# Optimization experiments

Hardware: AMD Instinct MI355X
Metric: run time of the kernel (lower is better)

The kernel has to match this reference:

```python
import jax, jax.numpy as jnp
import numpy as np

EMBED_DIM = 256
B, S = 4, 4096

def setup_inputs() -> dict:
    key = jax.random.key(0)
    k1, k2, k3, k4 = jax.random.split(key, 4)
    x = jax.random.normal(k1, (B, S, EMBED_DIM), dtype=jnp.float32)
    scale = 1.0 / np.sqrt(EMBED_DIM)
    Wq = jax.random.normal(k2, (EMBED_DIM, EMBED_DIM), dtype=jnp.float32) * scale
    Wk = jax.random.normal(k3, (EMBED_DIM, EMBED_DIM), dtype=jnp.float32) * scale
    Wv = jax.random.normal(k4, (EMBED_DIM, EMBED_DIM), dtype=jnp.float32) * scale
    return {"x": x, "Wq": Wq, "Wk": Wk, "Wv": Wv}

def reference(x, Wq, Wk, Wv):
    # nn.Linear: y = x @ W.T  (weights stored [out, in])
    Q = jnp.einsum('bse,oe->bso', x, Wq)
    K = jnp.einsum('bse,oe->bso', x, Wk)
    V = jnp.einsum('bse,oe->bso', x, Wv)
    inv_sqrt_d = 1.0 / np.sqrt(EMBED_DIM)
    scores = jnp.einsum('bqd,bkd->bqk', Q, K) * inv_sqrt_d  # [B,S,S]
    attn = jax.nn.softmax(scores, axis=-1)
    out = jnp.einsum('bqk,bkd->bqd', attn, V)
    return out
```

## Files before the change

kernel.cpp:

```cpp
#include <hip/hip_runtime.h>
#include <stdint.h>

#define SEQ   4096
#define EMB   256
#define NROW  16384

typedef short s16x8 __attribute__((ext_vector_type(8)));
typedef float f32x4 __attribute__((ext_vector_type(4)));

#define LOG2E 1.44269504088896340736f

__device__ __forceinline__ unsigned short f2bf(float f) {
    unsigned int u = __builtin_bit_cast(unsigned int, f);
    u += 0x7FFFu + ((u >> 16) & 1u);
    return (unsigned short)(u >> 16);
}

__device__ __forceinline__ void fence_barrier() {
    __asm__ volatile("s_waitcnt lgkmcnt(0)" ::: "memory");
    __builtin_amdgcn_s_barrier();
    __asm__ volatile("" ::: "memory");
}

__global__ __launch_bounds__(256, 8) void xcvt_kernel(
    const float* __restrict__ x, unsigned short* __restrict__ xb)
{
    const size_t i = (size_t)(blockIdx.x*256 + threadIdx.x) * 8;
    const float4 v0 = *(const float4*)(x + i);
    const float4 v1 = *(const float4*)(x + i + 4);
    union { unsigned short u[8]; s16x8 v; } o;
    o.u[0]=f2bf(v0.x); o.u[1]=f2bf(v0.y); o.u[2]=f2bf(v0.z); o.u[3]=f2bf(v0.w);
    o.u[4]=f2bf(v1.x); o.u[5]=f2bf(v1.y); o.u[6]=f2bf(v1.z); o.u[7]=f2bf(v1.w);
    *(s16x8*)(xb + i) = o.v;
}

#define PWSTR 264

__global__ __launch_bounds__(256, 2) void proj_kernel(
    const unsigned short* __restrict__ xb, const float* __restrict__ Wq,
    const float* __restrict__ Wk, const float* __restrict__ Wv,
    unsigned short* __restrict__ Qb, unsigned short* __restrict__ Kb,
    unsigned short* __restrict__ Vt)
{
    __shared__ unsigned short Wl[3][32][PWSTR];
    __shared__ unsigned short Vtr[32][72];
    const int bid = blockIdx.x;
    const int ct  = bid >> 6;
    const int rb  = bid & 63;
    const int t   = threadIdx.x;

    {
        const float* Ws[3] = {Wq, Wk, Wv};
        const int o = t >> 3, seg = t & 7;
        for (int w = 0; w < 3; ++w) {
            const float* src = Ws[w] + (ct*32 + o)*256 + seg*32;
            #pragma unroll
            for (int i = 0; i < 8; ++i) {
                float4 v = *(const float4*)(src + i*4);
                ushort4 bv;
                bv.x = f2bf(v.x); bv.y = f2bf(v.y); bv.z = f2bf(v.z); bv.w = f2bf(v.w);
                *(ushort4*)&Wl[w][o][seg*32 + i*4] = bv;
            }
        }
    }
    __syncthreads();

    const int wave = t >> 6, lane = t & 63;
    const int g = lane >> 4, lr = lane & 15;

    for (int it = 0; it < 4; ++it) {
        const int rowblk = rb*256 + it*64;
        const int rowbase = rowblk + wave*16;
        s16x8 a[8];
        {
            const unsigned short* xr = xb + (size_t)(rowbase + lr)*256;
            #pragma unroll
            for (int c = 0; c < 8; ++c)
                a[c] = *(const s16x8*)(xr + c*32 + g*8);
        }
        f32x4 acc[3][2];
        #pragma unroll
        for (int w = 0; w < 3; ++w)
            #pragma unroll
            for (int cf = 0; cf < 2; ++cf)
                #pragma unroll
                for (int j = 0; j < 4; ++j) acc[w][cf][j] = 0.0f;

        #pragma unroll
        for (int w = 0; w < 3; ++w)
            #pragma unroll
            for (int cf = 0; cf < 2; ++cf)
                #pragma unroll
                for (int c = 0; c < 8; ++c) {
                    s16x8 bfr = *(const s16x8*)&Wl[w][cf*16 + lr][c*32 + g*8];
                    acc[w][cf] = __builtin_amdgcn_mfma_f32_16x16x32_bf16(a[c], bfr, acc[w][cf], 0, 0, 0);
                }

        #pragma unroll
        for (int cf = 0; cf < 2; ++cf) {
            const int col = ct*32 + cf*16 + lr;
            #pragma unroll
            for (int j = 0; j < 4; ++j) {
                const int srow = rowbase + g*4 + j;
                Qb[(size_t)srow*256 + col] = f2bf(acc[0][cf][j] * 0.0625f);
                Kb[(size_t)srow*256 + col] = f2bf(acc[1][cf][j]);
            }
        }
        __syncthreads();
        #pragma unroll
        for (int cf = 0; cf < 2; ++cf) {
            ushort4 pv;
            pv.x = f2bf(acc[2][cf][0]); pv.y = f2bf(acc[2][cf][1]);
            pv.z = f2bf(acc[2][cf][2]); pv.w = f2bf(acc[2][cf][3]);
            *(ushort4*)&Vtr[cf*16 + lr][wave*16 + g*4] = pv;
        }
        __syncthreads();
        {
            const int colL = t >> 3, seg = t & 7;
            const int bb = rowblk >> 12, ss0 = rowblk & 4095;
            unsigned short* dst = Vt + ((size_t)(bb*256 + ct*32 + colL))*4096 + ss0 + seg*8;
            *(s16x8*)(dst) = *(const s16x8*)&Vtr[colL][seg*8];
        }
    }
}

#define KVB  32
#define NT   64
#define KSTR 264
#define VSTR 40
#define PSTR 40
#define RESCALE_THR 8.0f

__global__ __launch_bounds__(256, 2) void attn_kernel(
    const unsigned short* __restrict__ Qb, const unsigned short* __restrict__ Kb,
    const unsigned short* __restrict__ Vt, float* __restrict__ pacc0,
    float* __restrict__ pm, float* __restrict__ pl, float* __restrict__ out)
{
    __shared__ unsigned short Kl[2][KVB][KSTR];
    __shared__ unsigned short Vl[2][EMB][VSTR];
    __shared__ unsigned short Pl[4][16][PSTR];
    __shared__ float All[4][16];

    const int bid = blockIdx.x;
    const int grp = bid & 7;
    const int b = grp >> 1, h = grp & 1;
    const int qt  = bid >> 3;
    const int t   = threadIdx.x;
    const int wave = t >> 6, lane = t & 63;
    const int g = lane >> 4, lr = lane & 15;
    const int kv0 = h * 2048;
    const int rowbase = b*4096 + qt*64 + wave*16;

    s16x8 qa[8];
    {
        const unsigned short* qp = Qb + (size_t)(rowbase + lr)*256;
        #pragma unroll
        for (int c = 0; c < 8; ++c)
            qa[c] = *(const s16x8*)(qp + c*32 + g*8);
    }

    f32x4 acc[16];
    #pragma unroll
    for (int c = 0; c < 16; ++c)
        #pragma unroll
        for (int j = 0; j < 4; ++j) acc[c][j] = 0.0f;
    float m = -__builtin_inff(), l = 0.0f;

    const unsigned short* Kg = Kb + (size_t)b*4096*256;
    const unsigned short* Vg = Vt + (size_t)b*256*4096;

    s16x8 kreg[4], vreg[4];
    #pragma unroll
    for (int i = 0; i < 4; ++i) {
        const int idx = i*256 + t;
        const int kv = idx >> 5, e8 = idx & 31;
        kreg[i] = *(const s16x8*)(Kg + (size_t)(kv0 + kv)*256 + e8*8);
        const int d = idx >> 2, seg = idx & 3;
        vreg[i] = *(const s16x8*)(Vg + (size_t)d*4096 + kv0 + seg*8);
    }

    for (int kt = 0; kt < NT; ++kt) {
        const int buf = kt & 1;
        #pragma unroll
        for (int i = 0; i < 4; ++i) {
            const int idx = i*256 + t;
            const int kv = idx >> 5, e8 = idx & 31;
            *(s16x8*)&Kl[buf][kv][e8*8] = kreg[i];
            const int d = idx >> 2, seg = idx & 3;
            *(s16x8*)&Vl[buf][d][seg*8] = vreg[i];
        }
        if (kt + 1 < NT) {
            const int kvn = kv0 + (kt + 1) * KVB;
            #pragma unroll
            for (int i = 0; i < 4; ++i) {
                const int idx = i*256 + t;
                const int kv = idx >> 5, e8 = idx & 31;
                kreg[i] = *(const s16x8*)(Kg + (size_t)(kvn + kv)*256 + e8*8);
                const int d = idx >> 2, seg = idx & 3;
                vreg[i] = *(const s16x8*)(Vg + (size_t)d*4096 + kvn + seg*8);
            }
        }
        fence_barrier();

        f32x4 sc[2];
        #pragma unroll
        for (int f = 0; f < 2; ++f)
            #pragma unroll
            for (int j = 0; j < 4; ++j) sc[f][j] = 0.0f;
        __builtin_amdgcn_s_setprio(1);
        #pragma unroll
        for (int f = 0; f < 2; ++f)
            #pragma unroll
            for (int c = 0; c < 8; ++c) {
                s16x8 kb = *(const s16x8*)&Kl[buf][f*16 + lr][c*32 + g*8];
                sc[f] = __builtin_amdgcn_mfma_f32_16x16x32_bf16(kb, qa[c], sc[f], 0, 0, 0);
            }
        __builtin_amdgcn_s_setprio(0);

        float pmax = fmaxf(fmaxf(fmaxf(sc[0][0], sc[0][1]), fmaxf(sc[0][2], sc[0][3])),
                           fmaxf(fmaxf(sc[1][0], sc[1][1]), fmaxf(sc[1][2], sc[1][3])));
        pmax = fmaxf(pmax, __shfl_xor(pmax, 16));
        pmax = fmaxf(pmax, __shfl_xor(pmax, 32));

        if (!__all(pmax - m <= RESCALE_THR)) {
            const float mn = fmaxf(m, pmax);
            const float al = __builtin_amdgcn_exp2f((m - mn) * LOG2E);
            m = mn;
            l *= al;
            if (lane < 16) All[wave][lr] = al;
            f32x4 al4 = *(const f32x4*)&All[wave][g*4];
            #pragma unroll
            for (int c = 0; c < 16; ++c)
                #pragma unroll
                for (int j = 0; j < 4; ++j) acc[c][j] *= al4[j];
        }

        float p[2][4];
        #pragma unroll
        for (int f = 0; f < 2; ++f)
            #pragma unroll
            for (int j = 0; j < 4; ++j)
                p[f][j] = __builtin_amdgcn_exp2f((sc[f][j] - m) * LOG2E);
        float ps = (p[0][0] + p[0][1]) + (p[0][2] + p[0][3])
                 + (p[1][0] + p[1][1]) + (p[1][2] + p[1][3]);
        ps += __shfl_xor(ps, 16);
        ps += __shfl_xor(ps, 32);
        l += ps;

        ushort4 q0, q1;
        q0.x = f2bf(p[0][0]); q0.y = f2bf(p[0][1]); q0.z = f2bf(p[0][2]); q0.w = f2bf(p[0][3]);
        q1.x = f2bf(p[1][0]); q1.y = f2bf(p[1][1]); q1.z = f2bf(p[1][2]); q1.w = f2bf(p[1][3]);
        *(ushort4*)&Pl[wave][lr][g*4]      = q0;
        *(ushort4*)&Pl[wave][lr][16 + g*4] = q1;
        s16x8 pa = *(const s16x8*)&Pl[wave][lr][g*8];

        __builtin_amdgcn_s_setprio(1);
        #pragma unroll
        for (int c = 0; c < 16; ++c) {
            s16x8 vb = *(const s16x8*)&Vl[buf][c*16 + lr][g*8];
            acc[c] = __builtin_amdgcn_mfma_f32_16x16x32_bf16(pa, vb, acc[c], 0, 0, 0);
        }
        __builtin_amdgcn_s_setprio(0);
    }

    float* dst = h ? out : pacc0;
    #pragma unroll
    for (int c = 0; c < 16; ++c)
        #pragma unroll
        for (int j = 0; j < 4; ++j)
            dst[(size_t)(rowbase + g*4 + j)*256 + c*16 + lr] = acc[c][j];
    if (lane < 16) {
        pm[h*NROW + rowbase + lr] = m;
        pl[h*NROW + rowbase + lr] = l;
    }
}

__global__ __launch_bounds__(256, 4) void combine_kernel(
    const float* __restrict__ pacc0, const float* __restrict__ pm,
    const float* __restrict__ pl, float* __restrict__ out)
{
    const int idx = blockIdx.x*256 + threadIdx.x;
    const int row = idx >> 6, d4 = (idx & 63) << 2;
    const float m0 = pm[row], m1 = pm[NROW + row];
    const float l0 = pl[row], l1 = pl[NROW + row];
    const float M = fmaxf(m0, m1);
    const float w0 = __builtin_amdgcn_exp2f((m0 - M) * LOG2E);
    const float w1 = __builtin_amdgcn_exp2f((m1 - M) * LOG2E);
    const float r = 1.0f / (l0*w0 + l1*w1);
    const float4 a0 = *(const float4*)(pacc0 + (size_t)row*256 + d4);
    float4 a1 = *(const float4*)(out + (size_t)row*256 + d4);
    a1.x = (a0.x*w0 + a1.x*w1) * r;
    a1.y = (a0.y*w0 + a1.y*w1) * r;
    a1.z = (a0.z*w0 + a1.z*w1) * r;
    a1.w = (a0.w*w0 + a1.w*w1) * r;
    *(float4*)(out + (size_t)row*256 + d4) = a1;
}

extern "C" void kernel_launch(void* const* d_in, const int* in_sizes, int n_in,
                              void* d_out, int out_size, void* d_ws, size_t ws_size,
                              hipStream_t stream) {
    const float* x  = (const float*)d_in[0];
    const float* Wq = (const float*)d_in[1];
    const float* Wk = (const float*)d_in[2];
    const float* Wv = (const float*)d_in[3];

    unsigned short* Qb = (unsigned short*)d_ws;
    unsigned short* Kb = Qb + (size_t)NROW*EMB;
    unsigned short* Vt = Kb + (size_t)NROW*EMB;
    float* pacc0 = (float*)(Vt + (size_t)NROW*EMB);
    float* pm    = pacc0 + (size_t)NROW*EMB;
    float* pl    = pm + 2*NROW;
    unsigned short* xb = (unsigned short*)pacc0;

    xcvt_kernel<<<2048, 256, 0, stream>>>(x, xb);
    proj_kernel<<<512, 256, 0, stream>>>(xb, Wq, Wk, Wv, Qb, Kb, Vt);
    attn_kernel<<<512, 256, 0, stream>>>(Qb, Kb, Vt, pacc0, pm, pl, (float*)d_out);
    combine_kernel<<<4096, 256, 0, stream>>>(pacc0, pm, pl, (float*)d_out);
}
```

Measured before the change: 212.1 us.

## Rework attention to 32x32 MFMA with direct-to-LDS loads and intra-block KV split

The attention kernel moves to 512-thread blocks, each covering 128 query rows with 64-key tiles. Waves split the KV tile in half and merge their results in LDS at the end. It uses 32x32x16 bf16 MFMA, XOR-swizzled LDS staged through global_load_lds, and builds the P operand with cross-lane shuffles instead of an LDS round trip. The weight conversion to bf16 moves into the x-conversion kernel, and Q/K stores are coalesced through LDS in the projection kernel. The goals are fewer LDS round trips, fewer register-staged loads and better MFMA efficiency, at the cost of higher LDS use, a vmcnt(0) wait each tile and extra merge traffic.

```diff
diff --git a/kernel.cpp b/kernel.cpp
--- a/kernel.cpp
+++ b/kernel.cpp
@@ -5,10 +5,13 @@
 #define EMB   256
 #define NROW  16384
 
-typedef short s16x8 __attribute__((ext_vector_type(8)));
-typedef float f32x4 __attribute__((ext_vector_type(4)));
+typedef short s16x8  __attribute__((ext_vector_type(8)));
+typedef float f32x4  __attribute__((ext_vector_type(4)));
+typedef float f32x16 __attribute__((ext_vector_type(16)));
+typedef unsigned int u32;
 
 #define LOG2E 1.44269504088896340736f
+#define RESCALE_THR 8.0f
 
 __device__ __forceinline__ unsigned short f2bf(float f) {
     unsigned int u = __builtin_bit_cast(unsigned int, f);
@@ -16,33 +19,52 @@
     return (unsigned short)(u >> 16);
 }
 
-__device__ __forceinline__ void fence_barrier() {
-    __asm__ volatile("s_waitcnt lgkmcnt(0)" ::: "memory");
-    __builtin_amdgcn_s_barrier();
-    __asm__ volatile("" ::: "memory");
+__device__ __forceinline__ u32 pkbf2(float lo, float hi) {
+    return (u32)f2bf(lo) | ((u32)f2bf(hi) << 16);
+}
+
+typedef __attribute__((address_space(3))) u32 lds_u32;
+typedef __attribute__((address_space(1))) const u32 glb_u32;
+__device__ __forceinline__ void gload16(const unsigned short* g, const unsigned short* l) {
+    __builtin_amdgcn_global_load_lds((glb_u32*)(uintptr_t)g,
+                                     (lds_u32*)(u32)(uintptr_t)l, 16, 0, 0);
 }
 
 __global__ __launch_bounds__(256, 8) void xcvt_kernel(
-    const float* __restrict__ x, unsigned short* __restrict__ xb)
+    const float* __restrict__ x, const float* __restrict__ Wq,
+    const float* __restrict__ Wk, const float* __restrict__ Wv,
+    unsigned short* __restrict__ xb, unsigned short* __restrict__ Wb)
 {
-    const size_t i = (size_t)(blockIdx.x*256 + threadIdx.x) * 8;
-    const float4 v0 = *(const float4*)(x + i);
-    const float4 v1 = *(const float4*)(x + i + 4);
+    const int gid = blockIdx.x*256 + threadIdx.x;
+    const float* src;
+    unsigned short* dst;
+    size_t off;
+    if (gid < 524288) {
+        src = x; dst = xb; off = (size_t)gid * 8;
+    } else {
+        size_t wi = (size_t)(gid - 524288) * 8;
+        int w = (int)(wi >> 16);
+        off = wi & 65535;
+        src = (w == 0) ? Wq : (w == 1) ? Wk : Wv;
+        dst = Wb + (size_t)w * 65536;
+    }
+    const float4 v0 = *(const float4*)(src + off);
+    const float4 v1 = *(const float4*)(src + off + 4);
     union { unsigned short u[8]; s16x8 v; } o;
     o.u[0]=f2bf(v0.x); o.u[1]=f2bf(v0.y); o.u[2]=f2bf(v0.z); o.u[3]=f2bf(v0.w);
     o.u[4]=f2bf(v1.x); o.u[5]=f2bf(v1.y); o.u[6]=f2bf(v1.z); o.u[7]=f2bf(v1.w);
-    *(s16x8*)(xb + i) = o.v;
+    *(s16x8*)(dst + off) = o.v;
 }
 
 #define PWSTR 264
 
 __global__ __launch_bounds__(256, 2) void proj_kernel(
-    const unsigned short* __restrict__ xb, const float* __restrict__ Wq,
-    const float* __restrict__ Wk, const float* __restrict__ Wv,
+    const unsigned short* __restrict__ xb, const unsigned short* __restrict__ Wb,
     unsigned short* __restrict__ Qb, unsigned short* __restrict__ Kb,
     unsigned short* __restrict__ Vt)
 {
     __shared__ unsigned short Wl[3][32][PWSTR];
+    __shared__ unsigned short QKs[2][64][40];
     __shared__ unsigned short Vtr[32][72];
     const int bid = blockIdx.x;
     const int ct  = bid >> 6;
@@ -50,17 +72,13 @@
     const int t   = threadIdx.x;
 
     {
-        const float* Ws[3] = {Wq, Wk, Wv};
         const int o = t >> 3, seg = t & 7;
+        #pragma unroll
         for (int w = 0; w < 3; ++w) {
-            const float* src = Ws[w] + (ct*32 + o)*256 + seg*32;
-            #pragma unroll
-            for (int i = 0; i < 8; ++i) {
-                float4 v = *(const float4*)(src + i*4);
-                ushort4 bv;
-                bv.x = f2bf(v.x); bv.y = f2bf(v.y); bv.z = f2bf(v.z); bv.w = f2bf(v.w);
-                *(ushort4*)&Wl[w][o][seg*32 + i*4] = bv;
-            }
+            const unsigned short* src = Wb + (size_t)w*65536 + (ct*32 + o)*256 + seg*32;
+            #pragma unroll
+            for (int i = 0; i < 4; ++i)
+                *(s16x8*)&Wl[w][o][seg*32 + i*8] = *(const s16x8*)(src + i*8);
         }
     }
     __syncthreads();
@@ -96,19 +114,15 @@
                     acc[w][cf] = __builtin_amdgcn_mfma_f32_16x16x32_bf16(a[c], bfr, acc[w][cf], 0, 0, 0);
                 }
 
+        __syncthreads();
         #pragma unroll
         for (int cf = 0; cf < 2; ++cf) {
-            const int col = ct*32 + cf*16 + lr;
             #pragma unroll
             for (int j = 0; j < 4; ++j) {
-                const int srow = rowbase + g*4 + j;
-                Qb[(size_t)srow*256 + col] = f2bf(acc[0][cf][j] * 0.0625f);
-                Kb[(size_t)srow*256 + col] = f2bf(acc[1][cf][j]);
+                const int row = wave*16 + g*4 + j;
+                QKs[0][row][cf*16 + lr] = f2bf(acc[0][cf][j] * 0.0625f);
+                QKs[1][row][cf*16 + lr] = f2bf(acc[1][cf][j]);
             }
-        }
-        __syncthreads();
-        #pragma unroll
-        for (int cf = 0; cf < 2; ++cf) {
             ushort4 pv;
             pv.x = f2bf(acc[2][cf][0]); pv.y = f2bf(acc[2][cf][1]);
             pv.z = f2bf(acc[2][cf][2]); pv.w = f2bf(acc[2][cf][3]);
@@ -116,162 +130,190 @@
         }
         __syncthreads();
         {
+            const int row = t >> 2, cs = t & 3;
+            *(s16x8*)&Qb[(size_t)(rowblk + row)*256 + ct*32 + cs*8] = *(const s16x8*)&QKs[0][row][cs*8];
+            *(s16x8*)&Kb[(size_t)(rowblk + row)*256 + ct*32 + cs*8] = *(const s16x8*)&QKs[1][row][cs*8];
             const int colL = t >> 3, seg = t & 7;
             const int bb = rowblk >> 12, ss0 = rowblk & 4095;
-            unsigned short* dst = Vt + ((size_t)(bb*256 + ct*32 + colL))*4096 + ss0 + seg*8;
-            *(s16x8*)(dst) = *(const s16x8*)&Vtr[colL][seg*8];
-        }
-    }
-}
-
-#define KVB  32
-#define NT   64
-#define KSTR 264
-#define VSTR 40
-#define PSTR 40
-#define RESCALE_THR 8.0f
-
-__global__ __launch_bounds__(256, 2) void attn_kernel(
+            *(s16x8*)&Vt[((size_t)(bb*256 + ct*32 + colL))*4096 + ss0 + seg*8] = *(const s16x8*)&Vtr[colL][seg*8];
+        }
+    }
+}
+
+#define AKVB 64
+#define ANT  32
+
+__global__ __launch_bounds__(512, 2) void attn_kernel(
     const unsigned short* __restrict__ Qb, const unsigned short* __restrict__ Kb,
     const unsigned short* __restrict__ Vt, float* __restrict__ pacc0,
     float* __restrict__ pm, float* __restrict__ pl, float* __restrict__ out)
 {
-    __shared__ unsigned short Kl[2][KVB][KSTR];
-    __shared__ unsigned short Vl[2][EMB][VSTR];
-    __shared__ unsigned short Pl[4][16][PSTR];
-    __shared__ float All[4][16];
+    __shared__ unsigned short KV[65536];
+    __shared__ float All[8][32];
+    __shared__ float MrgM[128], MrgL[128], Wt1[128], Wt2[128];
 
     const int bid = blockIdx.x;
     const int grp = bid & 7;
     const int b = grp >> 1, h = grp & 1;
-    const int qt  = bid >> 3;
-    const int t   = threadIdx.x;
-    const int wave = t >> 6, lane = t & 63;
-    const int g = lane >> 4, lr = lane & 15;
+    const int qt = bid >> 3;
+    const int t = threadIdx.x;
+    const int w = t >> 6, lane = t & 63;
+    const int h8 = lane >> 5, lr5 = lane & 31;
+    const int qh = w >> 1, kvh = w & 1;
     const int kv0 = h * 2048;
-    const int rowbase = b*4096 + qt*64 + wave*16;
-
-    s16x8 qa[8];
-    {
-        const unsigned short* qp = Qb + (size_t)(rowbase + lr)*256;
-        #pragma unroll
-        for (int c = 0; c < 8; ++c)
-            qa[c] = *(const s16x8*)(qp + c*32 + g*8);
-    }
-
-    f32x4 acc[16];
-    #pragma unroll
-    for (int c = 0; c < 16; ++c)
-        #pragma unroll
-        for (int j = 0; j < 4; ++j) acc[c][j] = 0.0f;
-    float m = -__builtin_inff(), l = 0.0f;
+    const int rowbase = b*4096 + qt*128 + qh*32;
 
     const unsigned short* Kg = Kb + (size_t)b*4096*256;
     const unsigned short* Vg = Vt + (size_t)b*256*4096;
 
-    s16x8 kreg[4], vreg[4];
+    s16x8 qa[16];
+    {
+        const unsigned short* qp = Qb + (size_t)(rowbase + lr5)*256;
+        #pragma unroll
+        for (int mi = 0; mi < 16; ++mi)
+            qa[mi] = *(const s16x8*)(qp + mi*16 + h8*8);
+    }
+
+    f32x16 acc[8];
     #pragma unroll
-    for (int i = 0; i < 4; ++i) {
-        const int idx = i*256 + t;
-        const int kv = idx >> 5, e8 = idx & 31;
-        kreg[i] = *(const s16x8*)(Kg + (size_t)(kv0 + kv)*256 + e8*8);
-        const int d = idx >> 2, seg = idx & 3;
-        vreg[i] = *(const s16x8*)(Vg + (size_t)d*4096 + kv0 + seg*8);
-    }
-
-    for (int kt = 0; kt < NT; ++kt) {
+    for (int cc = 0; cc < 8; ++cc)
+        #pragma unroll
+        for (int r = 0; r < 16; ++r) acc[cc][r] = 0.0f;
+    float m = -__builtin_inff(), l = 0.0f;
+
+    auto stage = [&](int buf, int kt2) {
+        const int kvb = kv0 + kt2*AKVB;
+        #pragma unroll
+        for (int i = 0; i < 4; ++i) {
+            const int idx = i*512 + t;
+            const int kr = idx >> 5, ks = idx & 31;
+            gload16(Kg + (size_t)(kvb + kr)*256 + ((ks ^ (kr & 7)) << 3),
+                    &KV[buf*16384 + (idx << 3)]);
+            const int vr = idx >> 3, vs = idx & 7;
+            gload16(Vg + (size_t)vr*4096 + kvb + ((vs ^ (vr & 7)) << 3),
+                    &KV[32768 + buf*16384 + (idx << 3)]);
+        }
+    };
+
+    stage(0, 0);
+
+    for (int kt = 0; kt < ANT; ++kt) {
         const int buf = kt & 1;
-        #pragma unroll
-        for (int i = 0; i < 4; ++i) {
-            const int idx = i*256 + t;
-            const int kv = idx >> 5, e8 = idx & 31;
-            *(s16x8*)&Kl[buf][kv][e8*8] = kreg[i];
-            const int d = idx >> 2, seg = idx & 3;
-            *(s16x8*)&Vl[buf][d][seg*8] = vreg[i];
-        }
-        if (kt + 1 < NT) {
-            const int kvn = kv0 + (kt + 1) * KVB;
-            #pragma unroll
-            for (int i = 0; i < 4; ++i) {
-                const int idx = i*256 + t;
-                const int kv = idx >> 5, e8 = idx & 31;
-                kreg[i] = *(const s16x8*)(Kg + (size_t)(kvn + kv)*256 + e8*8);
-                const int d = idx >> 2, seg = idx & 3;
-                vreg[i] = *(const s16x8*)(Vg + (size_t)d*4096 + kvn + seg*8);
-            }
-        }
-        fence_barrier();
-
-        f32x4 sc[2];
-        #pragma unroll
-        for (int f = 0; f < 2; ++f)
-            #pragma unroll
-            for (int j = 0; j < 4; ++j) sc[f][j] = 0.0f;
+        __asm__ volatile("s_waitcnt vmcnt(0)" ::: "memory");
+        __builtin_amdgcn_s_barrier();
+        if (kt + 1 < ANT) stage(buf ^ 1, kt + 1);
+
+        const int krow = kvh*32 + lr5;
+        const int kbase = buf*16384 + krow*256;
+        const int ksw = krow & 7;
+        f32x16 sc;
+        #pragma unroll
+        for (int r = 0; r < 16; ++r) sc[r] = 0.0f;
         __builtin_amdgcn_s_setprio(1);
         #pragma unroll
-        for (int f = 0; f < 2; ++f)
-            #pragma unroll
-            for (int c = 0; c < 8; ++c) {
-                s16x8 kb = *(const s16x8*)&Kl[buf][f*16 + lr][c*32 + g*8];
-                sc[f] = __builtin_amdgcn_mfma_f32_16x16x32_bf16(kb, qa[c], sc[f], 0, 0, 0);
-            }
+        for (int mi = 0; mi < 16; ++mi) {
+            const int slot = (2*mi + h8) ^ ksw;
+            s16x8 kf = *(const s16x8*)&KV[kbase + slot*8];
+            sc = __builtin_amdgcn_mfma_f32_32x32x16_bf16(kf, qa[mi], sc, 0, 0, 0);
+        }
         __builtin_amdgcn_s_setprio(0);
 
-        float pmax = fmaxf(fmaxf(fmaxf(sc[0][0], sc[0][1]), fmaxf(sc[0][2], sc[0][3])),
-                           fmaxf(fmaxf(sc[1][0], sc[1][1]), fmaxf(sc[1][2], sc[1][3])));
-        pmax = fmaxf(pmax, __shfl_xor(pmax, 16));
+        float pmax = sc[0];
+        #pragma unroll
+        for (int r = 1; r < 16; ++r) pmax = fmaxf(pmax, sc[r]);
         pmax = fmaxf(pmax, __shfl_xor(pmax, 32));
 
         if (!__all(pmax - m <= RESCALE_THR)) {
             const float mn = fmaxf(m, pmax);
             const float al = __builtin_amdgcn_exp2f((m - mn) * LOG2E);
-            m = mn;
-            l *= al;
-            if (lane < 16) All[wave][lr] = al;
-            f32x4 al4 = *(const f32x4*)&All[wave][g*4];
-            #pragma unroll
-            for (int c = 0; c < 16; ++c)
+            m = mn; l *= al;
+            if (lane < 32) All[w][lr5] = al;
+            #pragma unroll
+            for (int rr = 0; rr < 4; ++rr) {
+                f32x4 a4 = *(const f32x4*)&All[w][rr*8 + 4*h8];
                 #pragma unroll
-                for (int j = 0; j < 4; ++j) acc[c][j] *= al4[j];
-        }
-
-        float p[2][4];
-        #pragma unroll
-        for (int f = 0; f < 2; ++f)
-            #pragma unroll
-            for (int j = 0; j < 4; ++j)
-                p[f][j] = __builtin_amdgcn_exp2f((sc[f][j] - m) * LOG2E);
-        float ps = (p[0][0] + p[0][1]) + (p[0][2] + p[0][3])
-                 + (p[1][0] + p[1][1]) + (p[1][2] + p[1][3]);
-        ps += __shfl_xor(ps, 16);
+                for (int rj = 0; rj < 4; ++rj)
+                    #pragma unroll
+                    for (int cc = 0; cc < 8; ++cc) acc[cc][rr*4 + rj] *= a4[rj];
+            }
+        }
+
+        #pragma unroll
+        for (int r = 0; r < 16; ++r) sc[r] = __builtin_amdgcn_exp2f((sc[r] - m) * LOG2E);
+        float ps = ((sc[0]+sc[1]) + (sc[2]+sc[3])) + ((sc[4]+sc[5]) + (sc[6]+sc[7]))
+                 + ((sc[8]+sc[9]) + (sc[10]+sc[11])) + ((sc[12]+sc[13]) + (sc[14]+sc[15]));
         ps += __shfl_xor(ps, 32);
         l += ps;
 
-        ushort4 q0, q1;
-        q0.x = f2bf(p[0][0]); q0.y = f2bf(p[0][1]); q0.z = f2bf(p[0][2]); q0.w = f2bf(p[0][3]);
-        q1.x = f2bf(p[1][0]); q1.y = f2bf(p[1][1]); q1.z = f2bf(p[1][2]); q1.w = f2bf(p[1][3]);
-        *(ushort4*)&Pl[wave][lr][g*4]      = q0;
-        *(ushort4*)&Pl[wave][lr][16 + g*4] = q1;
-        s16x8 pa = *(const s16x8*)&Pl[wave][lr][g*8];
-
+        const u32 dw0 = pkbf2(sc[0],  sc[1]),  dw1 = pkbf2(sc[2],  sc[3]);
+        const u32 dw2 = pkbf2(sc[4],  sc[5]),  dw3 = pkbf2(sc[6],  sc[7]);
+        const u32 dw4 = pkbf2(sc[8],  sc[9]),  dw5 = pkbf2(sc[10], sc[11]);
+        const u32 dw6 = pkbf2(sc[12], sc[13]), dw7 = pkbf2(sc[14], sc[15]);
+        const bool hi = (h8 != 0);
+        const u32 s10 = __shfl_xor(hi ? dw0 : dw2, 32);
+        const u32 s11 = __shfl_xor(hi ? dw1 : dw3, 32);
+        const u32 s20 = __shfl_xor(hi ? dw4 : dw6, 32);
+        const u32 s21 = __shfl_xor(hi ? dw5 : dw7, 32);
+        union { u32 u[4]; s16x8 v; } pa1, pa2;
+        pa1.u[0] = hi ? s10 : dw0;  pa1.u[1] = hi ? s11 : dw1;
+        pa1.u[2] = hi ? dw2 : s10;  pa1.u[3] = hi ? dw3 : s11;
+        pa2.u[0] = hi ? s20 : dw4;  pa2.u[1] = hi ? s21 : dw5;
+        pa2.u[2] = hi ? dw6 : s20;  pa2.u[3] = hi ? dw7 : s21;
+
+        const int vb0 = 32768 + buf*16384;
         __builtin_amdgcn_s_setprio(1);
         #pragma unroll
-        for (int c = 0; c < 16; ++c) {
-            s16x8 vb = *(const s16x8*)&Vl[buf][c*16 + lr][g*8];
-            acc[c] = __builtin_amdgcn_mfma_f32_16x16x32_bf16(pa, vb, acc[c], 0, 0, 0);
+        for (int cc = 0; cc < 8; ++cc) {
+            const int vrow = cc*32 + lr5;
+            const int vsw = vrow & 7;
+            s16x8 v1 = *(const s16x8*)&KV[vb0 + vrow*64 + (((4*kvh + h8)     ^ vsw) << 3)];
+            s16x8 v2 = *(const s16x8*)&KV[vb0 + vrow*64 + (((4*kvh + 2 + h8) ^ vsw) << 3)];
+            acc[cc] = __builtin_amdgcn_mfma_f32_32x32x16_bf16(pa1.v, v1, acc[cc], 0, 0, 0);
+            acc[cc] = __builtin_amdgcn_mfma_f32_32x32x16_bf16(pa2.v, v2, acc[cc], 0, 0, 0);
         }
         __builtin_amdgcn_s_setprio(0);
     }
 
-    float* dst = h ? out : pacc0;
-    #pragma unroll
-    for (int c = 0; c < 16; ++c)
-        #pragma unroll
-        for (int j = 0; j < 4; ++j)
-            dst[(size_t)(rowbase + g*4 + j)*256 + c*16 + lr] = acc[c][j];
-    if (lane < 16) {
-        pm[h*NROW + rowbase + lr] = m;
-        pl[h*NROW + rowbase + lr] = l;
+    __syncthreads();
+    float* Mrg = (float*)&KV[0];
+    if (kvh) {
+        #pragma unroll
+        for (int cc = 0; cc < 8; ++cc)
+            #pragma unroll
+            for (int r = 0; r < 16; ++r) {
+                const int qr = (r & 3) + 8*(r >> 2) + 4*h8;
+                Mrg[(qh*32 + qr)*256 + cc*32 + lr5] = acc[cc][r];
+            }
+        if (lane < 32) { MrgM[qh*32 + lr5] = m; MrgL[qh*32 + lr5] = l; }
+    }
+    __syncthreads();
+    if (!kvh) {
+        const float m2 = MrgM[qh*32 + lr5], l2 = MrgL[qh*32 + lr5];
+        const float M  = fmaxf(m, m2);
+        const float w1 = __builtin_amdgcn_exp2f((m  - M) * LOG2E);
+        const float w2 = __builtin_amdgcn_exp2f((m2 - M) * LOG2E);
+        const float lo = l*w1 + l2*w2;
+        if (lane < 32) {
+            Wt1[qh*32 + lr5] = w1; Wt2[qh*32 + lr5] = w2;
+            pm[h*NROW + rowbase + lr5] = M;
+            pl[h*NROW + rowbase + lr5] = lo;
+        }
+        float* dst = h ? out : pacc0;
+        #pragma unroll
+        for (int rr = 0; rr < 4; ++rr) {
+            f32x4 w1q = *(const f32x4*)&Wt1[qh*32 + rr*8 + 4*h8];
+            f32x4 w2q = *(const f32x4*)&Wt2[qh*32 + rr*8 + 4*h8];
+            #pragma unroll
+            for (int rj = 0; rj < 4; ++rj) {
+                const int qr = rj + 8*rr + 4*h8;
+                #pragma unroll
+                for (int cc = 0; cc < 8; ++cc) {
+                    const float v = acc[cc][rr*4 + rj]*w1q[rj]
+                                  + Mrg[(qh*32 + qr)*256 + cc*32 + lr5]*w2q[rj];
+                    dst[(size_t)(rowbase + qr)*256 + cc*32 + lr5] = v;
+                }
+            }
+        }
     }
 }
 
@@ -311,9 +353,10 @@
     float* pm    = pacc0 + (size_t)NROW*EMB;
     float* pl    = pm + 2*NROW;
     unsigned short* xb = (unsigned short*)pacc0;
-
-    xcvt_kernel<<<2048, 256, 0, stream>>>(x, xb);
-    proj_kernel<<<512, 256, 0, stream>>>(xb, Wq, Wk, Wv, Qb, Kb, Vt);
-    attn_kernel<<<512, 256, 0, stream>>>(Qb, Kb, Vt, pacc0, pm, pl, (float*)d_out);
+    unsigned short* Wb = xb + (size_t)NROW*EMB;
+
+    xcvt_kernel<<<2144, 256, 0, stream>>>(x, Wq, Wk, Wv, xb, Wb);
+    proj_kernel<<<512, 256, 0, stream>>>(xb, Wb, Qb, Kb, Vt);
+    attn_kernel<<<256, 512, 0, stream>>>(Qb, Kb, Vt, pacc0, pm, pl, (float*)d_out);
     combine_kernel<<<4096, 256, 0, stream>>>(pacc0, pm, pl, (float*)d_out);
 }
```

New measurement: 217.2 us. +2.4%, slower.
